# Optimization experiments

Hardware: AMD Instinct MI355X
Metric: run time of the kernel (lower is better)

The kernel has to match this reference:

```python
import jax, jax.numpy as jnp
import numpy as np


def setup_inputs() -> dict:
    key = jax.random.key(0)
    k1, k2 = jax.random.split(key)
    x = jax.random.normal(k1, (8, 16, 16, 16, 64), dtype=jnp.float32)
    gamma = jax.random.normal(k2, (1,), dtype=jnp.float32)
    return {"x": x, "gamma": gamma}


def reference(x, gamma):
    # x: (B, D, H, W, C); tokens N = D*H*W, head dim C
    B, D, H, W, C = x.shape
    N = D * H * W
    q = x.reshape(B, N, C)                          # proj_query (B, N, C)
    # energy = batch_dot(q, q^T) -> (B, N, N)
    energy = jnp.einsum('bnc,bmc->bnm', q, q)
    attn = jax.nn.softmax(energy, axis=-1)          # softmax over last axis
    out = jnp.einsum('bnm,bmc->bnc', attn, q)       # attend * V (V = q)
    out = out.reshape(B, D, H, W, C)
    return gamma * out + x                          # gamma-scaled residual
```

## Files before the change

### kernel.cpp

```cpp
#include <hip/hip_runtime.h>

typedef _Float16 f16;
typedef _Float16 f16x8 __attribute__((ext_vector_type(8)));
typedef _Float16 f16x4 __attribute__((ext_vector_type(4)));
typedef _Float16 f16x2 __attribute__((ext_vector_type(2)));
typedef float f32x16 __attribute__((ext_vector_type(16)));
typedef float f32x4 __attribute__((ext_vector_type(4)));
typedef unsigned int u32;
typedef u32 u32x2 __attribute__((ext_vector_type(2)));
typedef u32 u32x4v __attribute__((ext_vector_type(4)));

#define MFMA_F16 __builtin_amdgcn_mfma_f32_32x32x16_f16

constexpr int N    = 4096;
constexpr int C    = 64;
constexpr int KV   = 64;
constexpr int QB   = 128;
constexpr int NGRP = 2;
constexpr int NT2  = N / KV / NGRP;
constexpr float LOG2E = 1.44269504088896f;
constexpr float THR   = 11.0f;

__device__ __forceinline__ float fexp2(float x) {
#if __has_builtin(__builtin_amdgcn_exp2f)
    return __builtin_amdgcn_exp2f(x);
#else
    return __expf(x * 0.69314718055994531f);
#endif
}

__device__ __forceinline__ u32 pkrtz(float a, float b) {
    return __builtin_bit_cast(u32, __builtin_amdgcn_cvt_pkrtz(a, b));
}

__device__ __forceinline__ int swz8(int row, int bcol) {
    return row * 128 + (bcol ^ ((row & 15) << 3));
}

__device__ __forceinline__ f16x8 frag8(const char* base, int row, int bcol) {
    f16x4 lo = *(const f16x4*)(base + swz8(row, bcol));
    f16x4 hi = *(const f16x4*)(base + swz8(row, bcol + 8));
    return __builtin_shufflevector(lo, hi, 0, 1, 2, 3, 4, 5, 6, 7);
}

__global__ __launch_bounds__(512, 2)
void channel_attn_kernel(const float* __restrict__ x,
                         const float* __restrict__ gamma,
                         float* __restrict__ out) {
    __shared__ __align__(16) unsigned char smem[67584];

    const int tid = threadIdx.x;
    const int w   = tid >> 6;
    const int g   = w >> 2;
    const int qw  = w & 3;
    const int l   = tid & 63;
    const int h   = l >> 5;
    const int q   = l & 31;
    const int bid = blockIdx.x;
    const int b   = bid >> 5;
    const int qt  = bid & 31;
    const float* xb = x + (size_t)b * (N * C);
    const int qbase = qt * QB;
    const int qg = qw * 32 + q;

    const int qrow = qbase + qg;
    f16x8 Qf[4];
    {
        const float* qs = xb + (size_t)qrow * C + h * 8;
        #pragma unroll
        for (int kk = 0; kk < 4; ++kk) {
            f32x4 a  = *(const f32x4*)(qs + kk * 16);
            f32x4 c2 = *(const f32x4*)(qs + kk * 16 + 4);
            f16x8 f;
            f[0] = (f16)(a[0] * LOG2E);  f[1] = (f16)(a[1] * LOG2E);
            f[2] = (f16)(a[2] * LOG2E);  f[3] = (f16)(a[3] * LOG2E);
            f[4] = (f16)(c2[0] * LOG2E); f[5] = (f16)(c2[1] * LOG2E);
            f[6] = (f16)(c2[2] * LOG2E); f[7] = (f16)(c2[3] * LOG2E);
            Qf[kk] = f;
        }
    }

    const int sc = l;
    const int sg = qw;
    float stg[16];

    auto stage_load = [&](int kt) {
        const float* src = xb + ((size_t)((g * NT2 + kt) * KV + sg * 16) * C + sc);
        #pragma unroll
        for (int j = 0; j < 16; ++j) stg[j] = src[j * C];
    };
    auto stage_write = [&](int sel) {
        char* kb = (char*)smem + ((g << 1) | sel) * 16384;
        char* vb = kb + 8192;
        #pragma unroll
        for (int j = 0; j < 16; ++j)
            *(f16*)(kb + swz8(sg * 16 + j, sc * 2)) = (f16)stg[j];
        #pragma unroll
        for (int u = 0; u < 4; ++u) {
            u32x2 vv = { pkrtz(stg[4*u+0], stg[4*u+1]), pkrtz(stg[4*u+2], stg[4*u+3]) };
            *(u32x2*)(vb + swz8(sc, (sg * 16 + u * 4) * 2)) = vv;
        }
    };

    f32x16 ot[2] = {};
    float m_run = -INFINITY, l_run = 0.f;

    stage_load(0);
    stage_write(0);
    __syncthreads();

    int cur = 0;
    for (int kt = 0; kt < NT2; ++kt) {
        if (kt + 1 < NT2) stage_load(kt + 1);

        const char* kb = (const char*)smem + ((g << 1) | cur) * 16384;
        const char* vb = kb + 8192;

        f32x16 st[2];
        #pragma unroll
        for (int n = 0; n < 2; ++n) {
            f32x16 acc = {};
            #pragma unroll
            for (int kk = 0; kk < 4; ++kk) {
                f16x8 kf = frag8(kb, q + 32 * n, (kk * 16 + h * 8) * 2);
                acc = MFMA_F16(kf, Qf[kk], acc, 0, 0, 0);
            }
            st[n] = acc;
        }

        float mx[4];
        #pragma unroll
        for (int t = 0; t < 4; ++t) mx[t] = fmaxf(st[0][t], st[1][t]);
        #pragma unroll
        for (int r2 = 4; r2 < 16; r2 += 4)
            #pragma unroll
            for (int t = 0; t < 4; ++t)
                mx[t] = fmaxf(mx[t], fmaxf(st[0][r2 + t], st[1][r2 + t]));
        float pmax = fmaxf(fmaxf(mx[0], mx[1]), fmaxf(mx[2], mx[3]));
        pmax = fmaxf(pmax, __shfl_xor(pmax, 32, 64));

        if (!__all(pmax - m_run <= THR)) {
            float m_new = fmaxf(m_run, pmax);
            float scf = fexp2(m_run - m_new);
            l_run *= scf;
            #pragma unroll
            for (int mI = 0; mI < 2; ++mI)
                #pragma unroll
                for (int r2 = 0; r2 < 16; ++r2) ot[mI][r2] *= scf;
            m_run = m_new;
        }

        float rs4[4] = {0.f, 0.f, 0.f, 0.f};
        #pragma unroll
        for (int n = 0; n < 2; ++n)
            #pragma unroll
            for (int r2 = 0; r2 < 16; ++r2) {
                float p = fexp2(st[n][r2] - m_run);
                st[n][r2] = p;
                rs4[r2 & 3] += p;
            }
        float rs = (rs4[0] + rs4[1]) + (rs4[2] + rs4[3]);
        rs += __shfl_xor(rs, 32, 64);
        l_run += rs;

        f16x8 Pf[4];
        #pragma unroll
        for (int kk = 0; kk < 4; ++kk) {
            int n  = kk >> 1;
            int so = 2 * (kk & 1) + h;
            int sx = 2 * (kk & 1) + (1 - h);
            u32 ua0 = pkrtz(st[n][so*4+0], st[n][so*4+1]);
            u32 ua1 = pkrtz(st[n][so*4+2], st[n][so*4+3]);
            u32 ub0 = pkrtz(st[n][sx*4+0], st[n][sx*4+1]);
            u32 ub1 = pkrtz(st[n][sx*4+2], st[n][sx*4+3]);
            u32 r0 = __shfl_xor(ub0, 32, 64);
            u32 r1 = __shfl_xor(ub1, 32, 64);
            u32x4v uv;
            uv[0] = h ? r0 : ua0;
            uv[1] = h ? r1 : ua1;
            uv[2] = h ? ua0 : r0;
            uv[3] = h ? ua1 : r1;
            Pf[kk] = __builtin_bit_cast(f16x8, uv);
        }

        if (kt + 1 < NT2) stage_write(cur ^ 1);

        #pragma unroll
        for (int mI = 0; mI < 2; ++mI) {
            f32x16 acc = ot[mI];
            #pragma unroll
            for (int kk = 0; kk < 4; ++kk) {
                f16x8 vf = frag8(vb, q + 32 * mI, (kk * 16 + h * 8) * 2);
                acc = MFMA_F16(vf, Pf[kk], acc, 0, 0, 0);
            }
            ot[mI] = acc;
        }

        __syncthreads();
        cur ^= 1;
    }

    float* pO = (float*)smem;
    float* pm = (float*)(smem + 32768);
    float* pl = (float*)(smem + 33280);

    if (g == 1) {
        #pragma unroll
        for (int mI = 0; mI < 2; ++mI)
            #pragma unroll
            for (int r2 = 0; r2 < 16; ++r2) {
                int c = 32 * mI + (r2 & 3) + 8 * (r2 >> 2) + 4 * h;
                pO[c * 128 + qg] = ot[mI][r2];
            }
        if (h == 0) { pm[qg] = m_run; pl[qg] = l_run; }
    }
    __syncthreads();

    if (g == 0) {
        float m1 = pm[qg], l1 = pl[qg];
        float M  = fmaxf(m_run, m1);
        float a0 = fexp2(m_run - M);
        float a1 = fexp2(m1 - M);
        float invl = 1.0f / (l_run * a0 + l1 * a1);

        float* ep = (float*)(smem + 33792 + qw * 8448);
        #pragma unroll
        for (int mI = 0; mI < 2; ++mI)
            #pragma unroll
            for (int r2 = 0; r2 < 16; ++r2) {
                int c = 32 * mI + (r2 & 3) + 8 * (r2 >> 2) + 4 * h;
                float o = (ot[mI][r2] * a0 + pO[c * 128 + qg] * a1) * invl;
                ep[c * 33 + q] = o;
            }

        const float gm = gamma[0];
        float* ob = out + (size_t)b * (N * C);
        #pragma unroll
        for (int it = 0; it < 8; ++it) {
            int ql = it * 4 + (l >> 4);
            int c0 = (l & 15) * 4;
            f32x4 o;
            o[0] = ep[(c0 + 0) * 33 + ql];
            o[1] = ep[(c0 + 1) * 33 + ql];
            o[2] = ep[(c0 + 2) * 33 + ql];
            o[3] = ep[(c0 + 3) * 33 + ql];
            int row = qbase + qw * 32 + ql;
            f32x4 xi = *(const f32x4*)(xb + (size_t)row * C + c0);
            f32x4 res = { gm * o[0] + xi[0], gm * o[1] + xi[1],
                          gm * o[2] + xi[2], gm * o[3] + xi[3] };
            *(f32x4*)(ob + (size_t)row * C + c0) = res;
        }
    }
}

extern "C" void kernel_launch(void* const* d_in, const int* in_sizes, int n_in,
                              void* d_out, int out_size, void* d_ws, size_t ws_size,
                              hipStream_t stream) {
    const float* x     = (const float*)d_in[0];
    const float* gamma = (const float*)d_in[1];
    float* out         = (float*)d_out;
    dim3 grid(256), block(512);
    channel_attn_kernel<<<grid, block, 0, stream>>>(x, gamma, out);
}
```

Before: 207.5 us.

## Split KV range across four wave groups with 1024-thread blocks

Doubles the number of KV-split groups per block from two to four (1024 threads), so each group processes half as many KV tiles, and merges the four partial softmax states in shared memory. Staging loads become vectorized float4 row reads with packed fp16 stores for K and the transposed V. It adds setprio hints around the MFMA sections and remaps block ids so batch varies fastest. The trade-offs are a 128KB shared buffer, which limits occupancy to one block per CU, and extra merge and sync cost.

```diff
diff --git a/kernel.cpp b/kernel.cpp
--- a/kernel.cpp
+++ b/kernel.cpp
@@ -3,7 +3,6 @@
 typedef _Float16 f16;
 typedef _Float16 f16x8 __attribute__((ext_vector_type(8)));
 typedef _Float16 f16x4 __attribute__((ext_vector_type(4)));
-typedef _Float16 f16x2 __attribute__((ext_vector_type(2)));
 typedef float f32x16 __attribute__((ext_vector_type(16)));
 typedef float f32x4 __attribute__((ext_vector_type(4)));
 typedef unsigned int u32;
@@ -16,18 +15,12 @@
 constexpr int C    = 64;
 constexpr int KV   = 64;
 constexpr int QB   = 128;
-constexpr int NGRP = 2;
-constexpr int NT2  = N / KV / NGRP;
+constexpr int NGRP = 4;
+constexpr int NT4  = N / KV / NGRP;
 constexpr float LOG2E = 1.44269504088896f;
 constexpr float THR   = 11.0f;
 
-__device__ __forceinline__ float fexp2(float x) {
-#if __has_builtin(__builtin_amdgcn_exp2f)
-    return __builtin_amdgcn_exp2f(x);
-#else
-    return __expf(x * 0.69314718055994531f);
-#endif
-}
+__device__ __forceinline__ float fexp2(float x) { return __builtin_amdgcn_exp2f(x); }
 
 __device__ __forceinline__ u32 pkrtz(float a, float b) {
     return __builtin_bit_cast(u32, __builtin_amdgcn_cvt_pkrtz(a, b));
@@ -43,11 +36,11 @@
     return __builtin_shufflevector(lo, hi, 0, 1, 2, 3, 4, 5, 6, 7);
 }
 
-__global__ __launch_bounds__(512, 2)
+__global__ __launch_bounds__(1024, 4)
 void channel_attn_kernel(const float* __restrict__ x,
                          const float* __restrict__ gamma,
                          float* __restrict__ out) {
-    __shared__ __align__(16) unsigned char smem[67584];
+    __shared__ __align__(16) unsigned char smem[131072];
 
     const int tid = threadIdx.x;
     const int w   = tid >> 6;
@@ -57,13 +50,13 @@
     const int h   = l >> 5;
     const int q   = l & 31;
     const int bid = blockIdx.x;
-    const int b   = bid >> 5;
-    const int qt  = bid & 31;
+    const int b   = bid & 7;
+    const int qt  = bid >> 3;
     const float* xb = x + (size_t)b * (N * C);
     const int qbase = qt * QB;
-    const int qg = qw * 32 + q;
-
+    const int qg   = qw * 32 + q;
     const int qrow = qbase + qg;
+
     f16x8 Qf[4];
     {
         const float* qs = xb + (size_t)qrow * C + h * 8;
@@ -80,25 +73,27 @@
         }
     }
 
-    const int sc = l;
-    const int sg = qw;
-    float stg[16];
+    const int c0  = (l & 15) * 4;
+    const int kr0 = qw * 16 + (l >> 4) * 4;
+    f32x4 stg[4];
 
     auto stage_load = [&](int kt) {
-        const float* src = xb + ((size_t)((g * NT2 + kt) * KV + sg * 16) * C + sc);
-        #pragma unroll
-        for (int j = 0; j < 16; ++j) stg[j] = src[j * C];
+        const float* src = xb + ((size_t)((g * NT4 + kt) * KV + kr0) * C + c0);
+        #pragma unroll
+        for (int j = 0; j < 4; ++j) stg[j] = *(const f32x4*)(src + j * C);
     };
     auto stage_write = [&](int sel) {
-        char* kb = (char*)smem + ((g << 1) | sel) * 16384;
+        char* kb = (char*)smem + g * 32768 + sel * 16384;
         char* vb = kb + 8192;
         #pragma unroll
-        for (int j = 0; j < 16; ++j)
-            *(f16*)(kb + swz8(sg * 16 + j, sc * 2)) = (f16)stg[j];
-        #pragma unroll
-        for (int u = 0; u < 4; ++u) {
-            u32x2 vv = { pkrtz(stg[4*u+0], stg[4*u+1]), pkrtz(stg[4*u+2], stg[4*u+3]) };
-            *(u32x2*)(vb + swz8(sc, (sg * 16 + u * 4) * 2)) = vv;
+        for (int j = 0; j < 4; ++j) {
+            u32x2 kv2 = { pkrtz(stg[j][0], stg[j][1]), pkrtz(stg[j][2], stg[j][3]) };
+            *(u32x2*)(kb + swz8(kr0 + j, c0 * 2)) = kv2;
+        }
+        #pragma unroll
+        for (int i = 0; i < 4; ++i) {
+            u32x2 vv = { pkrtz(stg[0][i], stg[1][i]), pkrtz(stg[2][i], stg[3][i]) };
+            *(u32x2*)(vb + swz8(c0 + i, qw * 32 + (l >> 4) * 8)) = vv;
         }
     };
 
@@ -109,24 +104,27 @@
     stage_write(0);
     __syncthreads();
 
-    int cur = 0;
-    for (int kt = 0; kt < NT2; ++kt) {
-        if (kt + 1 < NT2) stage_load(kt + 1);
-
-        const char* kb = (const char*)smem + ((g << 1) | cur) * 16384;
+    #pragma unroll 2
+    for (int kt = 0; kt < NT4; ++kt) {
+        const int sel = kt & 1;
+        if (kt + 1 < NT4) stage_load(kt + 1);
+
+        const char* kb = (const char*)smem + g * 32768 + sel * 16384;
         const char* vb = kb + 8192;
 
         f32x16 st[2];
+        __builtin_amdgcn_s_setprio(1);
         #pragma unroll
         for (int n = 0; n < 2; ++n) {
             f32x16 acc = {};
             #pragma unroll
             for (int kk = 0; kk < 4; ++kk) {
-                f16x8 kf = frag8(kb, q + 32 * n, (kk * 16 + h * 8) * 2);
+                f16x8 kf = frag8(kb, q + 32 * n, kk * 32 + h * 16);
                 acc = MFMA_F16(kf, Qf[kk], acc, 0, 0, 0);
             }
             st[n] = acc;
         }
+        __builtin_amdgcn_s_setprio(0);
 
         float mx[4];
         #pragma unroll
@@ -183,72 +181,97 @@
             Pf[kk] = __builtin_bit_cast(f16x8, uv);
         }
 
-        if (kt + 1 < NT2) stage_write(cur ^ 1);
-
+        if (kt + 1 < NT4) stage_write(sel ^ 1);
+
+        __builtin_amdgcn_s_setprio(1);
         #pragma unroll
         for (int mI = 0; mI < 2; ++mI) {
             f32x16 acc = ot[mI];
             #pragma unroll
             for (int kk = 0; kk < 4; ++kk) {
-                f16x8 vf = frag8(vb, q + 32 * mI, (kk * 16 + h * 8) * 2);
+                f16x8 vf = frag8(vb, q + 32 * mI, kk * 32 + h * 16);
                 acc = MFMA_F16(vf, Pf[kk], acc, 0, 0, 0);
             }
             ot[mI] = acc;
         }
+        __builtin_amdgcn_s_setprio(0);
 
         __syncthreads();
-        cur ^= 1;
     }
 
     float* pO = (float*)smem;
-    float* pm = (float*)(smem + 32768);
-    float* pl = (float*)(smem + 33280);
-
-    if (g == 1) {
+    float* pm = (float*)(smem + 104448);
+    float* pl = pm + 384;
+
+    if (g > 0) {
+        float* po = pO + (size_t)(g - 1) * (128 * 68) + qg * 68;
+        #pragma unroll
+        for (int mI = 0; mI < 2; ++mI)
+            #pragma unroll
+            for (int j = 0; j < 4; ++j) {
+                f32x4 v = { ot[mI][4*j], ot[mI][4*j+1], ot[mI][4*j+2], ot[mI][4*j+3] };
+                *(f32x4*)(po + mI * 32 + j * 8 + h * 4) = v;
+            }
+        if (h == 0) { pm[(g - 1) * 128 + qg] = m_run; pl[(g - 1) * 128 + qg] = l_run; }
+    }
+    __syncthreads();
+
+    float L = 1.0f;
+    if (g == 0) {
+        float m1 = pm[qg], m2 = pm[128 + qg], m3 = pm[256 + qg];
+        float l1 = pl[qg], l2 = pl[128 + qg], l3 = pl[256 + qg];
+        float M  = fmaxf(fmaxf(m_run, m1), fmaxf(m2, m3));
+        float a0 = fexp2(m_run - M);
+        float ag[3] = { fexp2(m1 - M), fexp2(m2 - M), fexp2(m3 - M) };
+        L = l_run * a0 + l1 * ag[0] + l2 * ag[1] + l3 * ag[2];
+        #pragma unroll
+        for (int mI = 0; mI < 2; ++mI)
+            #pragma unroll
+            for (int r2 = 0; r2 < 16; ++r2) ot[mI][r2] *= a0;
+        #pragma unroll
+        for (int gg = 0; gg < 3; ++gg) {
+            const float* po = pO + (size_t)gg * (128 * 68) + qg * 68;
+            #pragma unroll
+            for (int mI = 0; mI < 2; ++mI)
+                #pragma unroll
+                for (int j = 0; j < 4; ++j) {
+                    f32x4 v = *(const f32x4*)(po + mI * 32 + j * 8 + h * 4);
+                    ot[mI][4*j+0] += ag[gg] * v[0];
+                    ot[mI][4*j+1] += ag[gg] * v[1];
+                    ot[mI][4*j+2] += ag[gg] * v[2];
+                    ot[mI][4*j+3] += ag[gg] * v[3];
+                }
+        }
+    }
+    __syncthreads();
+
+    if (g == 0) {
+        float invl = 1.0f / L;
+        float* ep = (float*)(smem + qw * 8448);
         #pragma unroll
         for (int mI = 0; mI < 2; ++mI)
             #pragma unroll
             for (int r2 = 0; r2 < 16; ++r2) {
                 int c = 32 * mI + (r2 & 3) + 8 * (r2 >> 2) + 4 * h;
-                pO[c * 128 + qg] = ot[mI][r2];
-            }
-        if (h == 0) { pm[qg] = m_run; pl[qg] = l_run; }
-    }
-    __syncthreads();
-
-    if (g == 0) {
-        float m1 = pm[qg], l1 = pl[qg];
-        float M  = fmaxf(m_run, m1);
-        float a0 = fexp2(m_run - M);
-        float a1 = fexp2(m1 - M);
-        float invl = 1.0f / (l_run * a0 + l1 * a1);
-
-        float* ep = (float*)(smem + 33792 + qw * 8448);
-        #pragma unroll
-        for (int mI = 0; mI < 2; ++mI)
-            #pragma unroll
-            for (int r2 = 0; r2 < 16; ++r2) {
-                int c = 32 * mI + (r2 & 3) + 8 * (r2 >> 2) + 4 * h;
-                float o = (ot[mI][r2] * a0 + pO[c * 128 + qg] * a1) * invl;
-                ep[c * 33 + q] = o;
+                ep[c * 33 + q] = ot[mI][r2] * invl;
             }
 
         const float gm = gamma[0];
         float* ob = out + (size_t)b * (N * C);
         #pragma unroll
         for (int it = 0; it < 8; ++it) {
-            int ql = it * 4 + (l >> 4);
-            int c0 = (l & 15) * 4;
+            int ql  = it * 4 + (l >> 4);
+            int cc0 = (l & 15) * 4;
             f32x4 o;
-            o[0] = ep[(c0 + 0) * 33 + ql];
-            o[1] = ep[(c0 + 1) * 33 + ql];
-            o[2] = ep[(c0 + 2) * 33 + ql];
-            o[3] = ep[(c0 + 3) * 33 + ql];
+            o[0] = ep[(cc0 + 0) * 33 + ql];
+            o[1] = ep[(cc0 + 1) * 33 + ql];
+            o[2] = ep[(cc0 + 2) * 33 + ql];
+            o[3] = ep[(cc0 + 3) * 33 + ql];
             int row = qbase + qw * 32 + ql;
-            f32x4 xi = *(const f32x4*)(xb + (size_t)row * C + c0);
+            f32x4 xi = *(const f32x4*)(xb + (size_t)row * C + cc0);
             f32x4 res = { gm * o[0] + xi[0], gm * o[1] + xi[1],
                           gm * o[2] + xi[2], gm * o[3] + xi[3] };
-            *(f32x4*)(ob + (size_t)row * C + c0) = res;
+            *(f32x4*)(ob + (size_t)row * C + cc0) = res;
         }
     }
 }
@@ -259,6 +282,6 @@
     const float* x     = (const float*)d_in[0];
     const float* gamma = (const float*)d_in[1];
     float* out         = (float*)d_out;
-    dim3 grid(256), block(512);
+    dim3 grid(256), block(1024);
     channel_attn_kernel<<<grid, block, 0, stream>>>(x, gamma, out);
 }
```

Result: slower. 349.4 us (+68.3%).
